# Kernel optimization log

Measured on AMD Instinct MI355X. Metric: run time of the kernel, lower is better.

The kernel has to match this reference:

```python
import jax, jax.numpy as jnp
import numpy as np

B, N, K = 2, 50000, 16
CIN, COUT, M = 64, 32, 4


def setup_inputs() -> dict:
    key = jax.random.key(0)
    ks = jax.random.split(key, 7)
    x = jax.random.normal(ks[0], (B, N, CIN), dtype=jnp.float32)
    adj = jax.random.randint(ks[1], (B, N, K), 0, N + 1)  # 0 == empty slot
    weight = jax.random.normal(ks[2], (M, COUT, CIN), dtype=jnp.float32) * 0.1
    bias = jax.random.normal(ks[3], (COUT,), dtype=jnp.float32) * 0.1
    u = jax.random.normal(ks[4], (M, CIN), dtype=jnp.float32) * 0.1
    v = jax.random.normal(ks[5], (M, CIN), dtype=jnp.float32) * 0.1
    c = jax.random.normal(ks[6], (M,), dtype=jnp.float32) * 0.1
    return {"x": x, "adj": adj, "weight": weight, "bias": bias,
            "u": u, "v": v, "c": c}


def _gather_padded(feat, adj):
    # feat: (B, N, ...); adj: (B, N, K) indices into zero-padded node axis
    # (index 0 selects the zero row, matching torch get_patches semantics)
    pad = jnp.zeros((feat.shape[0], 1) + feat.shape[2:], feat.dtype)
    feat_p = jnp.concatenate([pad, feat], axis=1)        # (B, N+1, ...)
    return jax.vmap(lambda f, a: f[a])(feat_p, adj)      # (B, N, K, ...)


def reference(x, adj, weight, bias, u, v, c):
    # degree normalization: 1/#nonzero-neighbors, 0 for isolated points
    deg = jnp.sum(adj != 0, axis=-1).astype(x.dtype)     # (B, N)
    inv_deg = jnp.where(deg != 0, 1.0 / deg, 0.0)        # (B, N)

    # mixture-kernel transform of every node, then neighbor gather
    wx = jnp.einsum('bnc,moc->bnmo', x, weight)          # (B, N, M, COUT)
    gathered = _gather_padded(wx, adj)                   # (B, N, K, M, COUT)

    # softmax-gated assignment q[b,n,k,m] = softmax_m(v.x_nbr + u.x_ctr + c)
    ux = jnp.einsum('mc,bnc->bnm', u, x)                 # (B, N, M)
    vx = jnp.einsum('mc,bnc->bnm', v, x)                 # (B, N, M)
    vg = _gather_padded(vx, adj)                         # (B, N, K, M)
    q = jax.nn.softmax(vg + ux[:, :, None, :] + c, axis=-1)

    # weighted sum over neighbors K and mixture components M
    out = jnp.einsum('bnkm,bnkmo->bno', q, gathered)     # (B, N, COUT)
    return out * inv_deg[..., None] + bias
```

## Files before the change

### kernel.cpp

```cpp
#include <hip/hip_runtime.h>

namespace {
constexpr int BB = 2;
constexpr int NN = 50000;
constexpr int KK = 16;
constexpr int CI = 64;
constexpr int CO = 32;
constexpr int MM = 4;
constexpr int BN = BB * NN;
constexpr int GROUPS = NN / 4;
constexpr int GRID = 768;
constexpr int WAVES = (GRID / 2) * 4;
}

typedef __attribute__((ext_vector_type(8))) short short8v;
typedef __attribute__((ext_vector_type(4))) float float4v;
typedef __attribute__((ext_vector_type(2))) float f32x2;

union F4P {
  float4 f4;
  f32x2 p[2];
};

__device__ __forceinline__ unsigned short bf16r(float f) {
  unsigned int u = __float_as_uint(f);
  u += 0x7FFFu + ((u >> 16) & 1u);
  return (unsigned short)(u >> 16);
}

__global__ __launch_bounds__(256) void k_prep(
    const float* __restrict__ x, const float* __restrict__ u,
    const float* __restrict__ v, float* __restrict__ ux,
    float* __restrict__ vx, unsigned short* __restrict__ xh) {
  int idx = blockIdx.x * 256 + threadIdx.x;
  if (idx >= BN) return;
  const float4* xr = (const float4*)(x + (size_t)idx * CI);
  float su[MM] = {0.f, 0.f, 0.f, 0.f};
  float sv[MM] = {0.f, 0.f, 0.f, 0.f};
  uint4 xpack[8];
#pragma unroll
  for (int t = 0; t < CI / 4; ++t) {
    float4 xv = xr[t];
#pragma unroll
    for (int m = 0; m < MM; ++m) {
      float4 uv = *(const float4*)(u + m * CI + t * 4);
      float4 vv = *(const float4*)(v + m * CI + t * 4);
      su[m] += uv.x * xv.x + uv.y * xv.y + uv.z * xv.z + uv.w * xv.w;
      sv[m] += vv.x * xv.x + vv.y * xv.y + vv.z * xv.z + vv.w * xv.w;
    }
    unsigned d0 = (unsigned)bf16r(xv.x) | ((unsigned)bf16r(xv.y) << 16);
    unsigned d1 = (unsigned)bf16r(xv.z) | ((unsigned)bf16r(xv.w) << 16);
    if (t & 1) {
      xpack[t >> 1].z = d0;
      xpack[t >> 1].w = d1;
    } else {
      xpack[t >> 1].x = d0;
      xpack[t >> 1].y = d1;
    }
  }
  ((float4*)ux)[idx] = make_float4(su[0], su[1], su[2], su[3]);
  ((float4*)vx)[idx] = make_float4(sv[0], sv[1], sv[2], sv[3]);
  uint4* xo = (uint4*)(xh + (size_t)idx * CI);
#pragma unroll
  for (int t = 0; t < 8; ++t) xo[t] = xpack[t];
}

__global__ __launch_bounds__(256, 3) void k_gather(
    const unsigned short* __restrict__ xh, const int* __restrict__ adj,
    const float* __restrict__ weight, const float* __restrict__ bias,
    const float* __restrict__ cvec, const float* __restrict__ ux,
    const float* __restrict__ vx, float* __restrict__ out) {
  __shared__ unsigned short w_lds[2 * 8 * 64 * 8];
  __shared__ unsigned short t_lds[4][8 * 256];
  __shared__ float q_lds[4][4][64];
  __shared__ float inv_lds[4][8];

  const int tid = threadIdx.x;
  const int lane = tid & 63;
  const int wv = tid >> 6;

  for (int i = tid; i < 2 * 8 * 64; i += 256) {
    int tl = i >> 9;
    int ks = (i >> 6) & 7;
    int l = i & 63;
    int o = tl * 16 + (l & 15);
    unsigned pk[4];
#pragma unroll
    for (int ee = 0; ee < 4; ++ee) {
      int k0 = ks * 32 + (l >> 4) * 8 + 2 * ee;
      unsigned lo = bf16r(weight[((k0 & 3) * CO + o) * CI + (k0 >> 2)]);
      unsigned hi =
          bf16r(weight[(((k0 + 1) & 3) * CO + o) * CI + ((k0 + 1) >> 2)]);
      pk[ee] = lo | (hi << 16);
    }
    *(uint4*)&w_lds[i * 8] = make_uint4(pk[0], pk[1], pk[2], pk[3]);
  }
  __syncthreads();

  const int m4 = lane & 3;
  const int k4 = lane >> 2;
  const float cm = cvec[m4];
  const float b0 = bias[lane & 15];
  const float b1 = bias[16 + (lane & 15)];

  const int xcd = blockIdx.x & 7;
  const int b = xcd >> 2;
  const int wb = ((blockIdx.x >> 3) << 2) | (xcd & 3);
  const int w = wb * 4 + wv;
  const size_t bbase = (size_t)b * NN;
  const unsigned short* xhb = xh + bbase * CI;
  const float* vxb = vx + bbase * MM;
  unsigned short* twv = t_lds[wv];

  int g = w;
  int av = 0;
  if (g < GROUPS) av = adj[(bbase + (size_t)g * 4) * KK + lane];
  int jrows = 0;
  int gbase = g;

#define LOADS(n, GV)                                                       \
  _Pragma("unroll") for (int k = 0; k < KK; ++k) {                         \
    int r = __builtin_amdgcn_readlane(av_c, (n)*16 + k);                   \
    const unsigned short* rp = xhb + (size_t)(max(r, 1) - 1) * CI;         \
    GV[k] = rp[lane];                                                      \
  }

#define ACC_NODE(n, GV)                                                    \
  {                                                                        \
    const float4* qp = (const float4*)&q_lds[wv][n][0];                    \
    f32x2 t01 = {0.f, 0.f}, t23 = {0.f, 0.f};                              \
    _Pragma("unroll") for (int k = 0; k < KK; ++k) {                       \
      float xv = __uint_as_float(GV[k] << 16);                             \
      F4P qv;                                                              \
      qv.f4 = qp[k];                                                       \
      t01 += qv.p[0] * xv;                                                 \
      t23 += qv.p[1] * xv;                                                 \
    }                                                                      \
    unsigned lo, hi;                                                       \
    asm("v_cvt_pk_bf16_f32 %0, %1, %2"                                     \
        : "=v"(lo)                                                         \
        : "v"(t01[0]), "v"(t01[1]));                                       \
    asm("v_cvt_pk_bf16_f32 %0, %1, %2"                                     \
        : "=v"(hi)                                                         \
        : "v"(t23[0]), "v"(t23[1]));                                       \
    int row = jrows * 4 + (n);                                             \
    unsigned boff = (unsigned)row * 512u +                                 \
                    (((unsigned)lane * 8u) ^ ((unsigned)(row & 7) << 4));  \
    *(uint2*)((char*)twv + boff) = make_uint2(lo, hi);                     \
  }

#define FLUSH(JC)                                                          \
  {                                                                        \
    float4v ac0 = {0.f, 0.f, 0.f, 0.f};                                    \
    float4v ac1 = {0.f, 0.f, 0.f, 0.f};                                    \
    const int arow = lane & 7;                                             \
    const unsigned axor = (unsigned)(arow & 7) << 4;                       \
    _Pragma("unroll") for (int ks = 0; ks < 8; ++ks) {                     \
      unsigned aoff =                                                      \
          (unsigned)arow * 512u +                                          \
          ((((unsigned)(lane >> 4)) * 16u + (unsigned)ks * 64u) ^ axor);   \
      short8v A = *(const short8v*)((const char*)twv + aoff);              \
      short8v Bl = *(const short8v*)&w_lds[(0 * 8 + ks) * 512 + lane * 8]; \
      short8v Bh = *(const short8v*)&w_lds[(1 * 8 + ks) * 512 + lane * 8]; \
      ac0 = __builtin_amdgcn_mfma_f32_16x16x32_bf16(A, Bl, ac0, 0, 0, 0);  \
      ac1 = __builtin_amdgcn_mfma_f32_16x16x32_bf16(A, Bh, ac1, 0, 0, 0);  \
    }                                                                      \
    int jj = lane >> 4;                                                    \
    int gg = gbase + jj * WAVES;                                           \
    if (jj < (JC) && gg < GROUPS) {                                        \
      float4 iv = *(const float4*)&inv_lds[wv][jj * 4];                    \
      float* op = out + (bbase + (size_t)gg * 4) * CO + (lane & 15);       \
      op[0] = ac0[0] * iv.x + b0;                                          \
      op[16] = ac1[0] * iv.x + b1;                                         \
      op[32] = ac0[1] * iv.y + b0;                                         \
      op[48] = ac1[1] * iv.y + b1;                                         \
      op[64] = ac0[2] * iv.z + b0;                                         \
      op[80] = ac1[2] * iv.z + b1;                                         \
      op[96] = ac0[3] * iv.w + b0;                                         \
      op[112] = ac1[3] * iv.w + b1;                                        \
    }                                                                      \
  }

  while (g < GROUPS) {
    const int av_c = av;
    const size_t bn0 = bbase + (size_t)g * 4;

    int as0 = __shfl(av_c, k4);
    int as1 = __shfl(av_c, 16 + k4);
    int as2 = __shfl(av_c, 32 + k4);
    int as3 = __shfl(av_c, 48 + k4);
    float vg0 = vxb[(size_t)(max(as0, 1) - 1) * MM + m4];
    float vg1 = vxb[(size_t)(max(as1, 1) - 1) * MM + m4];
    float vg2 = vxb[(size_t)(max(as2, 1) - 1) * MM + m4];
    float vg3 = vxb[(size_t)(max(as3, 1) - 1) * MM + m4];
    float ux0 = ux[bn0 * MM + m4];
    float ux1 = ux[(bn0 + 1) * MM + m4];
    float ux2 = ux[(bn0 + 2) * MM + m4];
    float ux3 = ux[(bn0 + 3) * MM + m4];
    const unsigned long long msk = __ballot(av_c != 0);

    unsigned gv0[KK], gv1[KK], gv2[KK], gv3[KK];
    LOADS(0, gv0)
    LOADS(1, gv1)
    LOADS(2, gv2)
    LOADS(3, gv3)

    const int gn = g + WAVES;
    if (gn < GROUPS) av = adj[(bbase + (size_t)gn * 4) * KK + lane];

    float i0, i1, i2, i3;
    {
      int d0 = __popc((unsigned)(msk & 0xFFFFull));
      int d1 = __popc((unsigned)((msk >> 16) & 0xFFFFull));
      int d2 = __popc((unsigned)((msk >> 32) & 0xFFFFull));
      int d3 = __popc((unsigned)((msk >> 48) & 0xFFFFull));
      i0 = d0 ? __builtin_amdgcn_rcpf((float)d0) : 0.f;
      i1 = d1 ? __builtin_amdgcn_rcpf((float)d1) : 0.f;
      i2 = d2 ? __builtin_amdgcn_rcpf((float)d2) : 0.f;
      i3 = d3 ? __builtin_amdgcn_rcpf((float)d3) : 0.f;
      float e0 = __expf(vg0 + ux0 + cm);
      float e1 = __expf(vg1 + ux1 + cm);
      float e2 = __expf(vg2 + ux2 + cm);
      float e3 = __expf(vg3 + ux3 + cm);
      float s0 = e0 + __shfl_xor(e0, 1);
      float s1 = e1 + __shfl_xor(e1, 1);
      float s2 = e2 + __shfl_xor(e2, 1);
      float s3 = e3 + __shfl_xor(e3, 1);
      s0 += __shfl_xor(s0, 2);
      s1 += __shfl_xor(s1, 2);
      s2 += __shfl_xor(s2, 2);
      s3 += __shfl_xor(s3, 2);
      q_lds[wv][0][lane] = (as0 != 0) ? e0 * __builtin_amdgcn_rcpf(s0) : 0.f;
      q_lds[wv][1][lane] = (as1 != 0) ? e1 * __builtin_amdgcn_rcpf(s1) : 0.f;
      q_lds[wv][2][lane] = (as2 != 0) ? e2 * __builtin_amdgcn_rcpf(s2) : 0.f;
      q_lds[wv][3][lane] = (as3 != 0) ? e3 * __builtin_amdgcn_rcpf(s3) : 0.f;
      if (lane == 0)
        *(float4*)&inv_lds[wv][jrows * 4] = make_float4(i0, i1, i2, i3);
    }

    ACC_NODE(0, gv0)
    ACC_NODE(1, gv1)
    ACC_NODE(2, gv2)
    ACC_NODE(3, gv3)

    ++jrows;
    g = gn;
    if (jrows == 2) {
      FLUSH(2)
      jrows = 0;
      gbase = g;
    }
  }
  if (jrows > 0) FLUSH(jrows)
}

__global__ __launch_bounds__(256) void k_uxvx(
    const float* __restrict__ x, const float* __restrict__ u,
    const float* __restrict__ v, float* __restrict__ ux,
    float* __restrict__ vx) {
  int idx = blockIdx.x * 256 + threadIdx.x;
  if (idx >= BN) return;
  const float4* xr = (const float4*)(x + (size_t)idx * CI);
  float su[MM] = {0.f, 0.f, 0.f, 0.f};
  float sv[MM] = {0.f, 0.f, 0.f, 0.f};
#pragma unroll
  for (int t = 0; t < CI / 4; ++t) {
    float4 xv = xr[t];
#pragma unroll
    for (int m = 0; m < MM; ++m) {
      float4 uv = *(const float4*)(u + m * CI + t * 4);
      float4 vv = *(const float4*)(v + m * CI + t * 4);
      su[m] += uv.x * xv.x + uv.y * xv.y + uv.z * xv.z + uv.w * xv.w;
      sv[m] += vv.x * xv.x + vv.y * xv.y + vv.z * xv.z + vv.w * xv.w;
    }
  }
  ((float4*)ux)[idx] = make_float4(su[0], su[1], su[2], su[3]);
  ((float4*)vx)[idx] = make_float4(sv[0], sv[1], sv[2], sv[3]);
}

__global__ __launch_bounds__(256) void k_main_old(
    const float* __restrict__ x, const int* __restrict__ adj,
    const float* __restrict__ weight, const float* __restrict__ bias,
    const float* __restrict__ cvec, const float* __restrict__ ux,
    const float* __restrict__ vx, float* __restrict__ out) {
  __shared__ float w_lds2[MM][CO][CI + 4];
  __shared__ float q_lds2[4][64];
  __shared__ float t_lds2[4][MM][CI];
  const int tid = threadIdx.x;
  const int lane = tid & 63;
  const int wv = tid >> 6;
#pragma unroll
  for (int i = 0; i < (MM * CO * CI) / 256; ++i) {
    int g = i * 256 + tid;
    w_lds2[g >> 11][(g >> 6) & (CO - 1)][g & (CI - 1)] = weight[g];
  }
  __syncthreads();
  const int k4 = lane >> 2;
  const int m4 = lane & 3;
  const int o = lane & 31;
  const int hh = lane >> 5;
  const float cm = cvec[m4];
  const float bo = bias[o];
  for (int g = blockIdx.x; g < BN / 4; g += gridDim.x) {
    const int bn = g * 4 + wv;
    const int b = (bn >= NN) ? 1 : 0;
    const int* adjp = adj + (size_t)bn * KK;
    const float* xb = x + (size_t)b * NN * CI;
    int4 A[4];
#pragma unroll
    for (int i = 0; i < 4; ++i) A[i] = ((const int4*)adjp)[i];
    int deg = 0;
#pragma unroll
    for (int i = 0; i < 4; ++i)
      deg += (A[i].x != 0) + (A[i].y != 0) + (A[i].z != 0) + (A[i].w != 0);
    const float inv_deg = (deg > 0) ? 1.0f / (float)deg : 0.0f;
    int a = adjp[k4];
    float vg = 0.f;
    if (a != 0) vg = vx[((size_t)b * NN + (a - 1)) * MM + m4];
    float logit = vg + ux[(size_t)bn * MM + m4] + cm;
    float mx = fmaxf(logit, __shfl_xor(logit, 1));
    mx = fmaxf(mx, __shfl_xor(mx, 2));
    float e = __expf(logit - mx);
    float s = e + __shfl_xor(e, 1);
    s += __shfl_xor(s, 2);
    q_lds2[wv][lane] = (a != 0) ? (e / s) : 0.f;
    int rows[KK];
    {
      int tmp[KK] = {A[0].x, A[0].y, A[0].z, A[0].w, A[1].x, A[1].y,
                     A[1].z, A[1].w, A[2].x, A[2].y, A[2].z, A[2].w,
                     A[3].x, A[3].y, A[3].z, A[3].w};
#pragma unroll
      for (int k = 0; k < KK; ++k) rows[k] = max(tmp[k], 1) - 1;
    }
    float xg[KK];
#pragma unroll
    for (int k = 0; k < KK; ++k) xg[k] = xb[(size_t)rows[k] * CI + lane];
    float t0 = 0.f, t1 = 0.f, t2 = 0.f, t3 = 0.f;
#pragma unroll
    for (int k = 0; k < KK; ++k) {
      float4 qv = *(const float4*)&q_lds2[wv][k * 4];
      t0 += qv.x * xg[k];
      t1 += qv.y * xg[k];
      t2 += qv.z * xg[k];
      t3 += qv.w * xg[k];
    }
    t_lds2[wv][0][lane] = t0;
    t_lds2[wv][1][lane] = t1;
    t_lds2[wv][2][lane] = t2;
    t_lds2[wv][3][lane] = t3;
    float a0 = 0.f, a1 = 0.f, a2 = 0.f, a3 = 0.f;
#pragma unroll
    for (int mm = 0; mm < 2; ++mm) {
      const float* wrow = &w_lds2[2 * hh + mm][o][0];
      const float* trow = &t_lds2[wv][2 * hh + mm][0];
#pragma unroll
      for (int t4 = 0; t4 < CI / 4; ++t4) {
        float4 wvv = *(const float4*)(wrow + 4 * t4);
        float4 tv = *(const float4*)(trow + 4 * t4);
        a0 += wvv.x * tv.x;
        a1 += wvv.y * tv.y;
        a2 += wvv.z * tv.z;
        a3 += wvv.w * tv.w;
      }
    }
    float acc = (a0 + a1) + (a2 + a3);
    acc += __shfl_xor(acc, 32);
    if (lane < 32) out[(size_t)bn * CO + o] = acc * inv_deg + bo;
  }
}

extern "C" void kernel_launch(void* const* d_in, const int* in_sizes, int n_in,
                              void* d_out, int out_size, void* d_ws,
                              size_t ws_size, hipStream_t stream) {
  const float* x = (const float*)d_in[0];
  const int* adj = (const int*)d_in[1];
  const float* weight = (const float*)d_in[2];
  const float* bias = (const float*)d_in[3];
  const float* u = (const float*)d_in[4];
  const float* v = (const float*)d_in[5];
  const float* cvec = (const float*)d_in[6];
  float* out = (float*)d_out;

  float* ux = (float*)d_ws;
  float* vx = ux + (size_t)BN * MM;
  const size_t base = (size_t)BN * MM * 2 * sizeof(float);
  const size_t xh_bytes = (size_t)BN * CI * sizeof(unsigned short);

  if (ws_size >= base + xh_bytes) {
    unsigned short* xhb = (unsigned short*)((char*)d_ws + base);
    k_prep<<<(BN + 255) / 256, 256, 0, stream>>>(x, u, v, ux, vx, xhb);
    k_gather<<<GRID, 256, 0, stream>>>(xhb, adj, weight, bias, cvec, ux, vx,
                                       out);
  } else {
    k_uxvx<<<(BN + 255) / 256, 256, 0, stream>>>(x, u, v, ux, vx);
    k_main_old<<<1024, 256, 0, stream>>>(x, adj, weight, bias, cvec, ux, vx,
                                         out);
  }
}
```

Before: 69.39 us.

## Double-buffer neighbor row gathers into LDS via async global_load_lds

Replaces the per-lane register gathers of neighbor feature rows with async global-to-LDS 16-byte loads into a per-wave double buffer. Loads for the next group are issued before the current group's softmax and accumulation and waited on with explicit vmcnt counts. Work is regrouped to 2 nodes per step, with 4 steps per MFMA flush. Grid and occupancy drop to 512 blocks at 2 per CU to make room for the larger LDS footprint. The hardcoded vmcnt(5) depends on the exact count of outstanding loads, so a compiler reordering could make the wait fragile.

```diff
diff --git a/kernel.cpp b/kernel.cpp
--- a/kernel.cpp
+++ b/kernel.cpp
@@ -8,8 +8,8 @@
 constexpr int CO = 32;
 constexpr int MM = 4;
 constexpr int BN = BB * NN;
-constexpr int GROUPS = NN / 4;
-constexpr int GRID = 768;
+constexpr int GROUPS2 = NN / 2;
+constexpr int GRID = 512;
 constexpr int WAVES = (GRID / 2) * 4;
 }
 
@@ -26,6 +26,12 @@
   unsigned int u = __float_as_uint(f);
   u += 0x7FFFu + ((u >> 16) & 1u);
   return (unsigned short)(u >> 16);
+}
+
+__device__ __forceinline__ void llds16(const void* g, void* l) {
+  __builtin_amdgcn_global_load_lds(
+      (const __attribute__((address_space(1))) unsigned int*)g,
+      (__attribute__((address_space(3))) unsigned int*)l, 16, 0, 0);
 }
 
 __global__ __launch_bounds__(256) void k_prep(
@@ -65,15 +71,16 @@
   for (int t = 0; t < 8; ++t) xo[t] = xpack[t];
 }
 
-__global__ __launch_bounds__(256, 3) void k_gather(
+__global__ __launch_bounds__(256, 2) void k_gather(
     const unsigned short* __restrict__ xh, const int* __restrict__ adj,
     const float* __restrict__ weight, const float* __restrict__ bias,
     const float* __restrict__ cvec, const float* __restrict__ ux,
     const float* __restrict__ vx, float* __restrict__ out) {
   __shared__ unsigned short w_lds[2 * 8 * 64 * 8];
   __shared__ unsigned short t_lds[4][8 * 256];
-  __shared__ float q_lds[4][4][64];
+  __shared__ float q_lds[4][2][64];
   __shared__ float inv_lds[4][8];
+  __shared__ __align__(16) char xbuf[4][2][32 * 128];
 
   const int tid = threadIdx.x;
   const int lane = tid & 63;
@@ -111,45 +118,21 @@
   const unsigned short* xhb = xh + bbase * CI;
   const float* vxb = vx + bbase * MM;
   unsigned short* twv = t_lds[wv];
-
-  int g = w;
-  int av = 0;
-  if (g < GROUPS) av = adj[(bbase + (size_t)g * 4) * KK + lane];
-  int jrows = 0;
-  int gbase = g;
-
-#define LOADS(n, GV)                                                       \
-  _Pragma("unroll") for (int k = 0; k < KK; ++k) {                         \
-    int r = __builtin_amdgcn_readlane(av_c, (n)*16 + k);                   \
-    const unsigned short* rp = xhb + (size_t)(max(r, 1) - 1) * CI;         \
-    GV[k] = rp[lane];                                                      \
-  }
-
-#define ACC_NODE(n, GV)                                                    \
+  char* xwv = &xbuf[wv][0][0];
+
+#define STAGE(B, AV)                                                       \
   {                                                                        \
-    const float4* qp = (const float4*)&q_lds[wv][n][0];                    \
-    f32x2 t01 = {0.f, 0.f}, t23 = {0.f, 0.f};                              \
-    _Pragma("unroll") for (int k = 0; k < KK; ++k) {                       \
-      float xv = __uint_as_float(GV[k] << 16);                             \
-      F4P qv;                                                              \
-      qv.f4 = qp[k];                                                       \
-      t01 += qv.p[0] * xv;                                                 \
-      t23 += qv.p[1] * xv;                                                 \
+    char* ldst = xwv + (B)*4096;                                           \
+    _Pragma("unroll") for (int li = 0; li < 4; ++li) {                     \
+      int e = li * 8 + (lane >> 3);                                        \
+      int rr = __shfl((AV), e);                                            \
+      unsigned r = (unsigned)(max(rr, 1) - 1);                             \
+      const char* ga = (const char*)xhb + (size_t)r * 128 + (lane & 7) * 16;\
+      llds16(ga, ldst + li * 1024);                                        \
     }                                                                      \
-    unsigned lo, hi;                                                       \
-    asm("v_cvt_pk_bf16_f32 %0, %1, %2"                                     \
-        : "=v"(lo)                                                         \
-        : "v"(t01[0]), "v"(t01[1]));                                       \
-    asm("v_cvt_pk_bf16_f32 %0, %1, %2"                                     \
-        : "=v"(hi)                                                         \
-        : "v"(t23[0]), "v"(t23[1]));                                       \
-    int row = jrows * 4 + (n);                                             \
-    unsigned boff = (unsigned)row * 512u +                                 \
-                    (((unsigned)lane * 8u) ^ ((unsigned)(row & 7) << 4));  \
-    *(uint2*)((char*)twv + boff) = make_uint2(lo, hi);                     \
-  }
-
-#define FLUSH(JC)                                                          \
+  }
+
+#define FLUSH(JR)                                                          \
   {                                                                        \
     float4v ac0 = {0.f, 0.f, 0.f, 0.f};                                    \
     float4v ac1 = {0.f, 0.f, 0.f, 0.f};                                    \
@@ -165,88 +148,111 @@
       ac0 = __builtin_amdgcn_mfma_f32_16x16x32_bf16(A, Bl, ac0, 0, 0, 0);  \
       ac1 = __builtin_amdgcn_mfma_f32_16x16x32_bf16(A, Bh, ac1, 0, 0, 0);  \
     }                                                                      \
-    int jj = lane >> 4;                                                    \
-    int gg = gbase + jj * WAVES;                                           \
-    if (jj < (JC) && gg < GROUPS) {                                        \
-      float4 iv = *(const float4*)&inv_lds[wv][jj * 4];                    \
-      float* op = out + (bbase + (size_t)gg * 4) * CO + (lane & 15);       \
-      op[0] = ac0[0] * iv.x + b0;                                          \
-      op[16] = ac1[0] * iv.x + b1;                                         \
-      op[32] = ac0[1] * iv.y + b0;                                         \
-      op[48] = ac1[1] * iv.y + b1;                                         \
-      op[64] = ac0[2] * iv.z + b0;                                         \
-      op[80] = ac1[2] * iv.z + b1;                                         \
-      op[96] = ac0[3] * iv.w + b0;                                         \
-      op[112] = ac1[3] * iv.w + b1;                                        \
+    const int jj = lane >> 4;                                              \
+    _Pragma("unroll") for (int ri = 0; ri < 4; ++ri) {                     \
+      int r = jj * 4 + ri;                                                 \
+      int gr = gbase + (r >> 1) * WAVES;                                   \
+      if (r < 2 * (JR) && gr < GROUPS2) {                                  \
+        float iv = inv_lds[wv][r];                                         \
+        size_t bn = bbase + (size_t)gr * 2 + (r & 1);                      \
+        out[bn * CO + (lane & 15)] = ac0[ri] * iv + b0;                    \
+        out[bn * CO + 16 + (lane & 15)] = ac1[ri] * iv + b1;               \
+      }                                                                    \
     }                                                                      \
   }
 
-  while (g < GROUPS) {
+  int g = w;
+  int av = 0;
+  if (g < GROUPS2) av = adj[(bbase + (size_t)g * 2) * KK + (lane & 31)];
+  if (g < GROUPS2) STAGE(0, av)
+  int gn = g + WAVES;
+  int av_n = 0;
+  if (gn < GROUPS2) av_n = adj[(bbase + (size_t)gn * 2) * KK + (lane & 31)];
+
+  int cur = 0;
+  int jrows = 0;
+  int gbase = g;
+
+  while (g < GROUPS2) {
     const int av_c = av;
-    const size_t bn0 = bbase + (size_t)g * 4;
+    const size_t bn0 = bbase + (size_t)g * 2;
 
     int as0 = __shfl(av_c, k4);
     int as1 = __shfl(av_c, 16 + k4);
-    int as2 = __shfl(av_c, 32 + k4);
-    int as3 = __shfl(av_c, 48 + k4);
     float vg0 = vxb[(size_t)(max(as0, 1) - 1) * MM + m4];
     float vg1 = vxb[(size_t)(max(as1, 1) - 1) * MM + m4];
-    float vg2 = vxb[(size_t)(max(as2, 1) - 1) * MM + m4];
-    float vg3 = vxb[(size_t)(max(as3, 1) - 1) * MM + m4];
     float ux0 = ux[bn0 * MM + m4];
     float ux1 = ux[(bn0 + 1) * MM + m4];
-    float ux2 = ux[(bn0 + 2) * MM + m4];
-    float ux3 = ux[(bn0 + 3) * MM + m4];
+
+    const int gnn = gn + WAVES;
+    int av_nn = 0;
+    if (gnn < GROUPS2)
+      av_nn = adj[(bbase + (size_t)gnn * 2) * KK + (lane & 31)];
+
+    const bool staged = (gn < GROUPS2);
+    if (staged) STAGE(cur ^ 1, av_n)
+
     const unsigned long long msk = __ballot(av_c != 0);
-
-    unsigned gv0[KK], gv1[KK], gv2[KK], gv3[KK];
-    LOADS(0, gv0)
-    LOADS(1, gv1)
-    LOADS(2, gv2)
-    LOADS(3, gv3)
-
-    const int gn = g + WAVES;
-    if (gn < GROUPS) av = adj[(bbase + (size_t)gn * 4) * KK + lane];
-
-    float i0, i1, i2, i3;
     {
       int d0 = __popc((unsigned)(msk & 0xFFFFull));
       int d1 = __popc((unsigned)((msk >> 16) & 0xFFFFull));
-      int d2 = __popc((unsigned)((msk >> 32) & 0xFFFFull));
-      int d3 = __popc((unsigned)((msk >> 48) & 0xFFFFull));
-      i0 = d0 ? __builtin_amdgcn_rcpf((float)d0) : 0.f;
-      i1 = d1 ? __builtin_amdgcn_rcpf((float)d1) : 0.f;
-      i2 = d2 ? __builtin_amdgcn_rcpf((float)d2) : 0.f;
-      i3 = d3 ? __builtin_amdgcn_rcpf((float)d3) : 0.f;
+      float i0 = d0 ? __builtin_amdgcn_rcpf((float)d0) : 0.f;
+      float i1 = d1 ? __builtin_amdgcn_rcpf((float)d1) : 0.f;
       float e0 = __expf(vg0 + ux0 + cm);
       float e1 = __expf(vg1 + ux1 + cm);
-      float e2 = __expf(vg2 + ux2 + cm);
-      float e3 = __expf(vg3 + ux3 + cm);
       float s0 = e0 + __shfl_xor(e0, 1);
       float s1 = e1 + __shfl_xor(e1, 1);
-      float s2 = e2 + __shfl_xor(e2, 1);
-      float s3 = e3 + __shfl_xor(e3, 1);
       s0 += __shfl_xor(s0, 2);
       s1 += __shfl_xor(s1, 2);
-      s2 += __shfl_xor(s2, 2);
-      s3 += __shfl_xor(s3, 2);
       q_lds[wv][0][lane] = (as0 != 0) ? e0 * __builtin_amdgcn_rcpf(s0) : 0.f;
       q_lds[wv][1][lane] = (as1 != 0) ? e1 * __builtin_amdgcn_rcpf(s1) : 0.f;
-      q_lds[wv][2][lane] = (as2 != 0) ? e2 * __builtin_amdgcn_rcpf(s2) : 0.f;
-      q_lds[wv][3][lane] = (as3 != 0) ? e3 * __builtin_amdgcn_rcpf(s3) : 0.f;
       if (lane == 0)
-        *(float4*)&inv_lds[wv][jrows * 4] = make_float4(i0, i1, i2, i3);
-    }
-
-    ACC_NODE(0, gv0)
-    ACC_NODE(1, gv1)
-    ACC_NODE(2, gv2)
-    ACC_NODE(3, gv3)
-
+        *(float2*)&inv_lds[wv][jrows * 2] = make_float2(i0, i1);
+    }
+
+    if (staged)
+      asm volatile("s_waitcnt vmcnt(5)" ::: "memory");
+    else
+      asm volatile("s_waitcnt vmcnt(0)" ::: "memory");
+
+    {
+      const char* xb = xwv + cur * 4096;
+      const int hn = lane >> 5;
+      const int c2 = lane & 31;
+      const float4* qp = (const float4*)&q_lds[wv][hn][0];
+      f32x2 a0 = {0.f, 0.f}, a1 = {0.f, 0.f};
+      f32x2 a2 = {0.f, 0.f}, a3 = {0.f, 0.f};
+#pragma unroll
+      for (int k = 0; k < KK; ++k) {
+        unsigned xx = *(const unsigned*)(xb + hn * 2048 + k * 128 + c2 * 4);
+        float xlo = __uint_as_float(xx << 16);
+        float xhi = __uint_as_float(xx & 0xFFFF0000u);
+        F4P q;
+        q.f4 = qp[k];
+        a0 += q.p[0] * xlo;
+        a1 += q.p[1] * xlo;
+        a2 += q.p[0] * xhi;
+        a3 += q.p[1] * xhi;
+      }
+      unsigned p0, p1, p2, p3;
+      asm("v_cvt_pk_bf16_f32 %0, %1, %2" : "=v"(p0) : "v"(a0[0]), "v"(a0[1]));
+      asm("v_cvt_pk_bf16_f32 %0, %1, %2" : "=v"(p1) : "v"(a1[0]), "v"(a1[1]));
+      asm("v_cvt_pk_bf16_f32 %0, %1, %2" : "=v"(p2) : "v"(a2[0]), "v"(a2[1]));
+      asm("v_cvt_pk_bf16_f32 %0, %1, %2" : "=v"(p3) : "v"(a3[0]), "v"(a3[1]));
+      int row = jrows * 2 + hn;
+      unsigned boff = (unsigned)row * 512u +
+                      (((unsigned)c2 * 16u) ^ ((unsigned)(row & 7) << 4));
+      *(uint4*)((char*)twv + boff) = make_uint4(p0, p1, p2, p3);
+    }
+
+    av = av_n;
+    av_n = av_nn;
+    g = gn;
+    gn = gnn;
+    cur ^= 1;
     ++jrows;
-    g = gn;
-    if (jrows == 2) {
-      FLUSH(2)
+    if (jrows == 4) {
+      FLUSH(4)
       jrows = 0;
       gbase = g;
     }
```

Result: no change. 69.53 us (+0.2%).

## Software-pipeline adjacency and softmax operand loads, fold degree scaling into q

Applied to the files above, without the earlier changes.

The gather loop now prefetches adjacency two groups ahead and loads the next group's vx/ux softmax operands one iteration early, so their latency overlaps the current group's row gathers and MFMA work. The per-node inverse degree is multiplied into the softmax weights instead of being staged in LDS and applied at flush, which removes the inv_lds buffer and its lane-0 store. Grid size and the occupancy hint in launch bounds are raised from 3 to 4 blocks. The extra live registers for the prefetched values may push against the tighter register budget that 4 blocks per CU imposes.

```diff
diff --git a/kernel.cpp b/kernel.cpp
--- a/kernel.cpp
+++ b/kernel.cpp
@@ -9,7 +9,7 @@
 constexpr int MM = 4;
 constexpr int BN = BB * NN;
 constexpr int GROUPS = NN / 4;
-constexpr int GRID = 768;
+constexpr int GRID = 1024;
 constexpr int WAVES = (GRID / 2) * 4;
 }
 
@@ -65,7 +65,7 @@
   for (int t = 0; t < 8; ++t) xo[t] = xpack[t];
 }
 
-__global__ __launch_bounds__(256, 3) void k_gather(
+__global__ __launch_bounds__(256, 4) void k_gather(
     const unsigned short* __restrict__ xh, const int* __restrict__ adj,
     const float* __restrict__ weight, const float* __restrict__ bias,
     const float* __restrict__ cvec, const float* __restrict__ ux,
@@ -73,7 +73,6 @@
   __shared__ unsigned short w_lds[2 * 8 * 64 * 8];
   __shared__ unsigned short t_lds[4][8 * 256];
   __shared__ float q_lds[4][4][64];
-  __shared__ float inv_lds[4][8];
 
   const int tid = threadIdx.x;
   const int lane = tid & 63;
@@ -111,12 +110,6 @@
   const unsigned short* xhb = xh + bbase * CI;
   const float* vxb = vx + bbase * MM;
   unsigned short* twv = t_lds[wv];
-
-  int g = w;
-  int av = 0;
-  if (g < GROUPS) av = adj[(bbase + (size_t)g * 4) * KK + lane];
-  int jrows = 0;
-  int gbase = g;
 
 #define LOADS(n, GV)                                                       \
   _Pragma("unroll") for (int k = 0; k < KK; ++k) {                         \
@@ -168,36 +161,47 @@
     int jj = lane >> 4;                                                    \
     int gg = gbase + jj * WAVES;                                           \
     if (jj < (JC) && gg < GROUPS) {                                        \
-      float4 iv = *(const float4*)&inv_lds[wv][jj * 4];                    \
       float* op = out + (bbase + (size_t)gg * 4) * CO + (lane & 15);       \
-      op[0] = ac0[0] * iv.x + b0;                                          \
-      op[16] = ac1[0] * iv.x + b1;                                         \
-      op[32] = ac0[1] * iv.y + b0;                                         \
-      op[48] = ac1[1] * iv.y + b1;                                         \
-      op[64] = ac0[2] * iv.z + b0;                                         \
-      op[80] = ac1[2] * iv.z + b1;                                         \
-      op[96] = ac0[3] * iv.w + b0;                                         \
-      op[112] = ac1[3] * iv.w + b1;                                        \
+      op[0] = ac0[0] + b0;                                                 \
+      op[16] = ac1[0] + b1;                                                \
+      op[32] = ac0[1] + b0;                                                \
+      op[48] = ac1[1] + b1;                                                \
+      op[64] = ac0[2] + b0;                                                \
+      op[80] = ac1[2] + b1;                                                \
+      op[96] = ac0[3] + b0;                                                \
+      op[112] = ac1[3] + b1;                                               \
     }                                                                      \
   }
+
+  int g = w;
+  int av = 0, av_n = 0;
+  int as0 = 0, as1 = 0, as2 = 0, as3 = 0;
+  float vg0 = 0.f, vg1 = 0.f, vg2 = 0.f, vg3 = 0.f;
+  float uxv0 = 0.f, uxv1 = 0.f, uxv2 = 0.f, uxv3 = 0.f;
+  if (g < GROUPS) {
+    av = adj[(bbase + (size_t)g * 4) * KK + lane];
+    as0 = __shfl(av, k4);
+    as1 = __shfl(av, 16 + k4);
+    as2 = __shfl(av, 32 + k4);
+    as3 = __shfl(av, 48 + k4);
+    vg0 = vxb[(size_t)(max(as0, 1) - 1) * MM + m4];
+    vg1 = vxb[(size_t)(max(as1, 1) - 1) * MM + m4];
+    vg2 = vxb[(size_t)(max(as2, 1) - 1) * MM + m4];
+    vg3 = vxb[(size_t)(max(as3, 1) - 1) * MM + m4];
+    const size_t bn0 = bbase + (size_t)g * 4;
+    uxv0 = ux[bn0 * MM + m4];
+    uxv1 = ux[(bn0 + 1) * MM + m4];
+    uxv2 = ux[(bn0 + 2) * MM + m4];
+    uxv3 = ux[(bn0 + 3) * MM + m4];
+  }
+  int gn = g + WAVES;
+  if (gn < GROUPS) av_n = adj[(bbase + (size_t)gn * 4) * KK + lane];
+
+  int jrows = 0;
+  int gbase = g;
 
   while (g < GROUPS) {
     const int av_c = av;
-    const size_t bn0 = bbase + (size_t)g * 4;
-
-    int as0 = __shfl(av_c, k4);
-    int as1 = __shfl(av_c, 16 + k4);
-    int as2 = __shfl(av_c, 32 + k4);
-    int as3 = __shfl(av_c, 48 + k4);
-    float vg0 = vxb[(size_t)(max(as0, 1) - 1) * MM + m4];
-    float vg1 = vxb[(size_t)(max(as1, 1) - 1) * MM + m4];
-    float vg2 = vxb[(size_t)(max(as2, 1) - 1) * MM + m4];
-    float vg3 = vxb[(size_t)(max(as3, 1) - 1) * MM + m4];
-    float ux0 = ux[bn0 * MM + m4];
-    float ux1 = ux[(bn0 + 1) * MM + m4];
-    float ux2 = ux[(bn0 + 2) * MM + m4];
-    float ux3 = ux[(bn0 + 3) * MM + m4];
-    const unsigned long long msk = __ballot(av_c != 0);
 
     unsigned gv0[KK], gv1[KK], gv2[KK], gv3[KK];
     LOADS(0, gv0)
@@ -205,23 +209,43 @@
     LOADS(2, gv2)
     LOADS(3, gv3)
 
-    const int gn = g + WAVES;
-    if (gn < GROUPS) av = adj[(bbase + (size_t)gn * 4) * KK + lane];
-
-    float i0, i1, i2, i3;
+    const int gnn = gn + WAVES;
+    int av_nn = 0;
+    if (gnn < GROUPS) av_nn = adj[(bbase + (size_t)gnn * 4) * KK + lane];
+
+    int nas0 = 0, nas1 = 0, nas2 = 0, nas3 = 0;
+    float nvg0 = 0.f, nvg1 = 0.f, nvg2 = 0.f, nvg3 = 0.f;
+    float nux0 = 0.f, nux1 = 0.f, nux2 = 0.f, nux3 = 0.f;
+    if (gn < GROUPS) {
+      nas0 = __shfl(av_n, k4);
+      nas1 = __shfl(av_n, 16 + k4);
+      nas2 = __shfl(av_n, 32 + k4);
+      nas3 = __shfl(av_n, 48 + k4);
+      nvg0 = vxb[(size_t)(max(nas0, 1) - 1) * MM + m4];
+      nvg1 = vxb[(size_t)(max(nas1, 1) - 1) * MM + m4];
+      nvg2 = vxb[(size_t)(max(nas2, 1) - 1) * MM + m4];
+      nvg3 = vxb[(size_t)(max(nas3, 1) - 1) * MM + m4];
+      const size_t bnn = bbase + (size_t)gn * 4;
+      nux0 = ux[bnn * MM + m4];
+      nux1 = ux[(bnn + 1) * MM + m4];
+      nux2 = ux[(bnn + 2) * MM + m4];
+      nux3 = ux[(bnn + 3) * MM + m4];
+    }
+
     {
+      const unsigned long long msk = __ballot(av_c != 0);
       int d0 = __popc((unsigned)(msk & 0xFFFFull));
       int d1 = __popc((unsigned)((msk >> 16) & 0xFFFFull));
       int d2 = __popc((unsigned)((msk >> 32) & 0xFFFFull));
       int d3 = __popc((unsigned)((msk >> 48) & 0xFFFFull));
-      i0 = d0 ? __builtin_amdgcn_rcpf((float)d0) : 0.f;
-      i1 = d1 ? __builtin_amdgcn_rcpf((float)d1) : 0.f;
-      i2 = d2 ? __builtin_amdgcn_rcpf((float)d2) : 0.f;
-      i3 = d3 ? __builtin_amdgcn_rcpf((float)d3) : 0.f;
-      float e0 = __expf(vg0 + ux0 + cm);
-      float e1 = __expf(vg1 + ux1 + cm);
-      float e2 = __expf(vg2 + ux2 + cm);
-      float e3 = __expf(vg3 + ux3 + cm);
+      float i0 = d0 ? __builtin_amdgcn_rcpf((float)d0) : 0.f;
+      float i1 = d1 ? __builtin_amdgcn_rcpf((float)d1) : 0.f;
+      float i2 = d2 ? __builtin_amdgcn_rcpf((float)d2) : 0.f;
+      float i3 = d3 ? __builtin_amdgcn_rcpf((float)d3) : 0.f;
+      float e0 = __expf(vg0 + uxv0 + cm);
+      float e1 = __expf(vg1 + uxv1 + cm);
+      float e2 = __expf(vg2 + uxv2 + cm);
+      float e3 = __expf(vg3 + uxv3 + cm);
       float s0 = e0 + __shfl_xor(e0, 1);
       float s1 = e1 + __shfl_xor(e1, 1);
       float s2 = e2 + __shfl_xor(e2, 1);
@@ -230,12 +254,14 @@
       s1 += __shfl_xor(s1, 2);
       s2 += __shfl_xor(s2, 2);
       s3 += __shfl_xor(s3, 2);
-      q_lds[wv][0][lane] = (as0 != 0) ? e0 * __builtin_amdgcn_rcpf(s0) : 0.f;
-      q_lds[wv][1][lane] = (as1 != 0) ? e1 * __builtin_amdgcn_rcpf(s1) : 0.f;
-      q_lds[wv][2][lane] = (as2 != 0) ? e2 * __builtin_amdgcn_rcpf(s2) : 0.f;
-      q_lds[wv][3][lane] = (as3 != 0) ? e3 * __builtin_amdgcn_rcpf(s3) : 0.f;
-      if (lane == 0)
-        *(float4*)&inv_lds[wv][jrows * 4] = make_float4(i0, i1, i2, i3);
+      q_lds[wv][0][lane] =
+          (as0 != 0) ? e0 * __builtin_amdgcn_rcpf(s0) * i0 : 0.f;
+      q_lds[wv][1][lane] =
+          (as1 != 0) ? e1 * __builtin_amdgcn_rcpf(s1) * i1 : 0.f;
+      q_lds[wv][2][lane] =
+          (as2 != 0) ? e2 * __builtin_amdgcn_rcpf(s2) * i2 : 0.f;
+      q_lds[wv][3][lane] =
+          (as3 != 0) ? e3 * __builtin_amdgcn_rcpf(s3) * i3 : 0.f;
     }
 
     ACC_NODE(0, gv0)
@@ -244,12 +270,28 @@
     ACC_NODE(3, gv3)
 
     ++jrows;
-    g = gn;
     if (jrows == 2) {
       FLUSH(2)
       jrows = 0;
-      gbase = g;
-    }
+      gbase = gn;
+    }
+
+    g = gn;
+    gn = gnn;
+    av = av_n;
+    av_n = av_nn;
+    as0 = nas0;
+    as1 = nas1;
+    as2 = nas2;
+    as3 = nas3;
+    vg0 = nvg0;
+    vg1 = nvg1;
+    vg2 = nvg2;
+    vg3 = nvg3;
+    uxv0 = nux0;
+    uxv1 = nux1;
+    uxv2 = nux2;
+    uxv3 = nux3;
   }
   if (jrows > 0) FLUSH(jrows)
 }
```

After: 74.69 us. +7.6%, slower.
